# Performance work log

Hardware: AMD Instinct MI355X
Metric: run time of the kernel (lower is better)

## Reference

```python
import jax, jax.numpy as jnp
import numpy as np

B, L, C = 16, 4096, 9          # batch, max chars, max candidate spans per char (2+3+4)
DI, DO, V = 512, 128, 96       # char hidden, attention/pos-embed dim, pos-BEM vocab


def setup_inputs() -> dict:
    key = jax.random.key(0)
    k0, k1, k2, k3, k4, k5 = jax.random.split(key, 6)
    input_context = jax.random.normal(k0, (B, L, DI), jnp.float32)
    W = jax.random.normal(k1, (DO, DI), jnp.float32) / np.sqrt(DI).astype(np.float32)
    pos_embed = jax.random.normal(k2, (V, DO), jnp.float32)
    cand_idx = jax.random.randint(k3, (B, L, C), 0, V, dtype=jnp.int32)
    cand_mask = jax.random.randint(k4, (B, L, C), 0, 2, dtype=jnp.int32).astype(bool)
    word_seq_len = jax.random.randint(k5, (B,), L // 2, L + 1, dtype=jnp.int32)
    return {
        'input_context': input_context,
        'W': W,
        'pos_embed': pos_embed,
        'cand_idx': cand_idx,
        'cand_mask': cand_mask,
        'word_seq_len': word_seq_len,
    }


def reference(input_context, W, pos_embed, cand_idx, cand_mask, word_seq_len):
    # 'general' attention: score_c = cand_c . (W x_char)
    q = jnp.einsum('bld,od->blo', input_context, W)          # [B, L, DO]
    cand = pos_embed[cand_idx]                               # [B, L, C, DO] gather
    scores = jnp.einsum('blco,blo->blc', cand, q)            # [B, L, C]
    neg = jnp.finfo(scores.dtype).min
    attn = jax.nn.softmax(jnp.where(cand_mask, scores, neg), axis=-1)
    ctx = jnp.einsum('blc,blco->blo', attn, cand)            # [B, L, DO]
    # chars with no matched candidate -> zeros(output_size); pad beyond seq_len -> zeros
    has_cand = cand_mask.any(axis=-1, keepdims=True)         # [B, L, 1]
    in_len = jnp.arange(L, dtype=word_seq_len.dtype)[None, :, None] < word_seq_len[:, None, None]
    return jnp.where(has_cand & in_len, ctx, jnp.zeros((), ctx.dtype))
```

## Files before the change

kernel.cpp:

```cpp
#include <hip/hip_runtime.h>
#include <hip/hip_bf16.h>
#include <hip/hip_fp16.h>
#include <cfloat>

#define BB   16
#define LL   4096
#define CC   9
#define DIN  512
#define DOUT 128
#define VV   96

#define PWLD 520
#define PELD 136

typedef _Float16 h2 __attribute__((ext_vector_type(2)));

#if defined(__has_builtin)
#if __has_builtin(__builtin_amdgcn_fdot2)
#define FDOT2(a, b, c) __builtin_amdgcn_fdot2((a), (b), (c), false)
#endif
#endif
#ifndef FDOT2
__device__ __forceinline__ float FDOT2(h2 a, h2 b, float c) {
    return c + (float)a[0] * (float)b[0] + (float)a[1] * (float)b[1];
}
#endif

__device__ __forceinline__ h2 pack_h2(float lo, float hi) {
    return __builtin_bit_cast(h2, __builtin_amdgcn_cvt_pkrtz(lo, hi));
}

__global__ __launch_bounds__(128)
void pw_kernel(const float* __restrict__ W,
               const float* __restrict__ PE,
               __half*      __restrict__ PW,
               __half*      __restrict__ PEh)
{
    const int v = blockIdx.x;
    const int k = blockIdx.y * 128 + threadIdx.x;
    const float* per = PE + v * DOUT;
    float a = 0.f;
    #pragma unroll 8
    for (int o = 0; o < DOUT; ++o)
        a = fmaf(per[o], W[(size_t)o * DIN + k], a);
    PW[(size_t)v * DIN + k] = __float2half_rn(a);
    if (blockIdx.y == 0)
        PEh[(size_t)v * DOUT + threadIdx.x] = __float2half_rn(per[threadIdx.x]);
}

__global__ __launch_bounds__(1024)
void attn_kernel(const float*  __restrict__ X,
                 const __half* __restrict__ PW,
                 const __half* __restrict__ PEh,
                 const int*    __restrict__ CIDX,
                 const int*    __restrict__ CMASK,
                 const int*    __restrict__ SLEN,
                 float*        __restrict__ OUT)
{
    __shared__ __half lds_pw[VV * PWLD];
    __shared__ __half lds_pe[VV * PELD];

    const int t = threadIdx.x;

    #pragma unroll
    for (int it = 0; it < 6; ++it) {
        int chunk = t + it * 1024;
        int v = chunk >> 6, kq = chunk & 63;
        uint4 d = *(const uint4*)(PW + (size_t)v * DIN + kq * 8);
        *(uint4*)&lds_pw[v * PWLD + kq * 8] = d;
    }
    {
        if (t < 1536) {
            int v = t >> 4, kq = t & 15;
            *(uint4*)&lds_pe[v * PELD + kq * 8] =
                *(const uint4*)(PEh + (size_t)v * DOUT + kq * 8);
        }
        int c2 = t + 1024;
        if (c2 < 1536) {
            int v2 = c2 >> 4, k2 = c2 & 15;
            *(uint4*)&lds_pe[v2 * PELD + k2 * 8] =
                *(const uint4*)(PEh + (size_t)v2 * DOUT + k2 * 8);
        }
    }
    __syncthreads();

    const int lane = t & 63;
    const int il   = lane & 15;
    const int slot = t >> 4;
    const int rowbase = blockIdx.x * 128;

    #pragma unroll
    for (int iter = 0; iter < 2; ++iter) {
        const int row = rowbase + iter * 64 + slot;
        const int  b     = row >> 12;
        const int  l     = row & (LL - 1);
        const bool inlen = l < SLEN[b];

        int ci[CC], vm[CC];
        #pragma unroll
        for (int c = 0; c < CC; ++c) ci[c]  = CIDX[(size_t)row * CC + c];
        #pragma unroll
        for (int c = 0; c < CC; ++c) vm[c] = CMASK[(size_t)row * CC + c];
        int anym = 0;
        #pragma unroll
        for (int c = 0; c < CC; ++c) anym |= vm[c];
        const bool alive = inlen && (anym != 0);

        float* op = OUT + (size_t)row * DOUT + il * 8;

        if (!alive) {
            *(float4*)op       = make_float4(0.f, 0.f, 0.f, 0.f);
            *(float4*)(op + 4) = make_float4(0.f, 0.f, 0.f, 0.f);
        } else {
            const float* xr = X + (size_t)row * DIN;
            float4 xf[8];
            #pragma unroll
            for (int j = 0; j < 4; ++j) {
                xf[j * 2 + 0] = *(const float4*)(xr + il * 8 + 128 * j);
                xf[j * 2 + 1] = *(const float4*)(xr + il * 8 + 128 * j + 4);
            }
            h2 xh[16];
            #pragma unroll
            for (int q = 0; q < 8; ++q) {
                xh[q * 2 + 0] = pack_h2(xf[q].x, xf[q].y);
                xh[q * 2 + 1] = pack_h2(xf[q].z, xf[q].w);
            }

            float sc[CC];
            #pragma unroll
            for (int c = 0; c < CC; ++c) sc[c] = 0.f;
            #pragma unroll
            for (int j = 0; j < 4; ++j) {
                #pragma unroll
                for (int c = 0; c < CC; ++c) {
                    uint4 pwb = *(const uint4*)&lds_pw[ci[c] * PWLD + j * 128 + il * 8];
                    h2 p0 = __builtin_bit_cast(h2, pwb.x);
                    h2 p1 = __builtin_bit_cast(h2, pwb.y);
                    h2 p2 = __builtin_bit_cast(h2, pwb.z);
                    h2 p3 = __builtin_bit_cast(h2, pwb.w);
                    float s = sc[c];
                    s = FDOT2(xh[j * 4 + 0], p0, s);
                    s = FDOT2(xh[j * 4 + 1], p1, s);
                    s = FDOT2(xh[j * 4 + 2], p2, s);
                    s = FDOT2(xh[j * 4 + 3], p3, s);
                    sc[c] = s;
                }
            }
            #pragma unroll
            for (int c = 0; c < CC; ++c) {
                float s = sc[c];
                s += __shfl_xor(s, 1);
                s += __shfl_xor(s, 2);
                s += __shfl_xor(s, 4);
                s += __shfl_xor(s, 8);
                sc[c] = s;
            }

            float mx = -FLT_MAX;
            #pragma unroll
            for (int c = 0; c < CC; ++c)
                if (vm[c]) mx = fmaxf(mx, sc[c]);
            float e[CC], den = 0.f;
            #pragma unroll
            for (int c = 0; c < CC; ++c) {
                e[c] = vm[c] ? __expf(sc[c] - mx) : 0.f;
                den += e[c];
            }
            const float scale = 1.f / den;

            float o[8];
            #pragma unroll
            for (int j = 0; j < 8; ++j) o[j] = 0.f;
            #pragma unroll
            for (int c = 0; c < CC; ++c) {
                const float w = e[c];
                uint4 peb = *(const uint4*)&lds_pe[ci[c] * PELD + il * 8];
                h2 q0 = __builtin_bit_cast(h2, peb.x);
                h2 q1 = __builtin_bit_cast(h2, peb.y);
                h2 q2 = __builtin_bit_cast(h2, peb.z);
                h2 q3 = __builtin_bit_cast(h2, peb.w);
                o[0] = fmaf(w, (float)q0[0], o[0]); o[1] = fmaf(w, (float)q0[1], o[1]);
                o[2] = fmaf(w, (float)q1[0], o[2]); o[3] = fmaf(w, (float)q1[1], o[3]);
                o[4] = fmaf(w, (float)q2[0], o[4]); o[5] = fmaf(w, (float)q2[1], o[5]);
                o[6] = fmaf(w, (float)q3[0], o[6]); o[7] = fmaf(w, (float)q3[1], o[7]);
            }

            *(float4*)op       = make_float4(o[0] * scale, o[1] * scale, o[2] * scale, o[3] * scale);
            *(float4*)(op + 4) = make_float4(o[4] * scale, o[5] * scale, o[6] * scale, o[7] * scale);
        }
    }
}

extern "C" void kernel_launch(void* const* d_in, const int* in_sizes, int n_in,
                              void* d_out, int out_size, void* d_ws, size_t ws_size,
                              hipStream_t stream) {
    const float* X  = (const float*)d_in[0];
    const float* W  = (const float*)d_in[1];
    const float* PE = (const float*)d_in[2];
    const int*   CI = (const int*)d_in[3];
    const int*   CM = (const int*)d_in[4];
    const int*   SL = (const int*)d_in[5];
    float* OUT = (float*)d_out;
    __half* PW  = (__half*)d_ws;
    __half* PEh = (__half*)d_ws + (size_t)VV * DIN;

    hipLaunchKernelGGL(pw_kernel, dim3(VV, 4), dim3(128), 0, stream, W, PE, PW, PEh);

    const int rows = BB * LL;
    hipLaunchKernelGGL(attn_kernel, dim3(rows / 128), dim3(1024), 0, stream,
                       X, PW, PEh, CI, CM, SL, OUT);
}
```

Before: 40.85 us.

## Shrink LDS footprint: cache part of PW table, read rest and PE from global

The LDS copy of the projected table is cut to the first 76 vocabulary rows, and the PE table is no longer staged in LDS. Rows at or above 76 and all PE rows are read from global memory, relying on cache. The smaller LDS footprint (~79KB versus ~125KB) is meant to allow two workgroups per CU and less staging work per block. In exchange, some loads become divergent global loads inside the inner loop, which adds latency and branch divergence.

```diff
diff --git a/kernel.cpp b/kernel.cpp
--- a/kernel.cpp
+++ b/kernel.cpp
@@ -11,7 +11,7 @@
 #define VV   96
 
 #define PWLD 520
-#define PELD 136
+#define LDSV 76
 
 typedef _Float16 h2 __attribute__((ext_vector_type(2)));
 
@@ -43,12 +43,12 @@
     #pragma unroll 8
     for (int o = 0; o < DOUT; ++o)
         a = fmaf(per[o], W[(size_t)o * DIN + k], a);
-    PW[(size_t)v * DIN + k] = __float2half_rn(a);
+    PW[(size_t)v * PWLD + k] = __float2half_rn(a);
     if (blockIdx.y == 0)
         PEh[(size_t)v * DOUT + threadIdx.x] = __float2half_rn(per[threadIdx.x]);
 }
 
-__global__ __launch_bounds__(1024)
+__global__ __launch_bounds__(1024, 8)
 void attn_kernel(const float*  __restrict__ X,
                  const __half* __restrict__ PW,
                  const __half* __restrict__ PEh,
@@ -57,29 +57,17 @@
                  const int*    __restrict__ SLEN,
                  float*        __restrict__ OUT)
 {
-    __shared__ __half lds_pw[VV * PWLD];
-    __shared__ __half lds_pe[VV * PELD];
+    __shared__ __half lds_pw[LDSV * PWLD];
 
     const int t = threadIdx.x;
 
     #pragma unroll
-    for (int it = 0; it < 6; ++it) {
+    for (int it = 0; it < 5; ++it) {
         int chunk = t + it * 1024;
-        int v = chunk >> 6, kq = chunk & 63;
-        uint4 d = *(const uint4*)(PW + (size_t)v * DIN + kq * 8);
-        *(uint4*)&lds_pw[v * PWLD + kq * 8] = d;
-    }
-    {
-        if (t < 1536) {
-            int v = t >> 4, kq = t & 15;
-            *(uint4*)&lds_pe[v * PELD + kq * 8] =
-                *(const uint4*)(PEh + (size_t)v * DOUT + kq * 8);
-        }
-        int c2 = t + 1024;
-        if (c2 < 1536) {
-            int v2 = c2 >> 4, k2 = c2 & 15;
-            *(uint4*)&lds_pe[v2 * PELD + k2 * 8] =
-                *(const uint4*)(PEh + (size_t)v2 * DOUT + k2 * 8);
+        if (chunk < LDSV * 64) {
+            int v = chunk >> 6, kq = chunk & 63;
+            *(uint4*)&lds_pw[v * PWLD + kq * 8] =
+                *(const uint4*)(PW + (size_t)v * PWLD + kq * 8);
         }
     }
     __syncthreads();
@@ -133,7 +121,10 @@
             for (int j = 0; j < 4; ++j) {
                 #pragma unroll
                 for (int c = 0; c < CC; ++c) {
-                    uint4 pwb = *(const uint4*)&lds_pw[ci[c] * PWLD + j * 128 + il * 8];
+                    const int off = ci[c] * PWLD + j * 128 + il * 8;
+                    uint4 pwb;
+                    if (ci[c] < LDSV) pwb = *(const uint4*)&lds_pw[off];
+                    else              pwb = *(const uint4*)(PW + off);
                     h2 p0 = __builtin_bit_cast(h2, pwb.x);
                     h2 p1 = __builtin_bit_cast(h2, pwb.y);
                     h2 p2 = __builtin_bit_cast(h2, pwb.z);
@@ -174,7 +165,7 @@
             #pragma unroll
             for (int c = 0; c < CC; ++c) {
                 const float w = e[c];
-                uint4 peb = *(const uint4*)&lds_pe[ci[c] * PELD + il * 8];
+                uint4 peb = *(const uint4*)(PEh + (size_t)ci[c] * DOUT + il * 8);
                 h2 q0 = __builtin_bit_cast(h2, peb.x);
                 h2 q1 = __builtin_bit_cast(h2, peb.y);
                 h2 q2 = __builtin_bit_cast(h2, peb.z);
@@ -202,7 +193,7 @@
     const int*   SL = (const int*)d_in[5];
     float* OUT = (float*)d_out;
     __half* PW  = (__half*)d_ws;
-    __half* PEh = (__half*)d_ws + (size_t)VV * DIN;
+    __half* PEh = (__half*)((char*)d_ws + 99840);
 
     hipLaunchKernelGGL(pw_kernel, dim3(VV, 4), dim3(128), 0, stream, W, PE, PW, PEh);
 
```

Result: slower. 56.64 us (+38.6%).
